# Optimization experiments

Hardware: AMD Instinct MI355X
Metric: run time of the kernel (lower is better)

The kernel has to match this reference:

```python
import jax, jax.numpy as jnp
import numpy as np

B, S, D = 4, 4096, 256
NEG_INF = jnp.float32(-jnp.inf)


def setup_inputs() -> dict:
    key = jax.random.key(0)
    ks = jax.random.split(key, 6)
    x_q = jax.random.normal(ks[0], (B, S, D), dtype=jnp.float32)
    x_k = jax.random.normal(ks[1], (B, S, D), dtype=jnp.float32)
    x_v = jax.random.normal(ks[2], (B, S, D), dtype=jnp.float32)
    attn_mask = jnp.ones((B, S), dtype=jnp.int32)
    # Linear(d_model, d_model, bias=False) weights, torch layout [out, in]
    sc = 1.0 / np.sqrt(D)
    Wq = jax.random.uniform(ks[3], (D, D), minval=-sc, maxval=sc, dtype=jnp.float32)
    Wk = jax.random.uniform(ks[4], (D, D), minval=-sc, maxval=sc, dtype=jnp.float32)
    Wv = jax.random.uniform(ks[5], (D, D), minval=-sc, maxval=sc, dtype=jnp.float32)
    return {"x_q": x_q, "x_k": x_k, "x_v": x_v, "attn_mask": attn_mask,
            "Wq": Wq, "Wk": Wk, "Wv": Wv}


def reference(x_q, x_k, x_v, attn_mask, Wq, Wk, Wv):
    # projections: torch Linear -> x @ W.T
    Q = jnp.einsum('bsd,ed->bse', x_q, Wq)
    K = jnp.einsum('bsd,ed->bse', x_k, Wk)
    V = jnp.einsum('bsd,ed->bse', x_v, Wv)
    d = Q.shape[-1]
    n_q, n_k = Q.shape[1], K.shape[1]
    scale = jnp.sqrt(jnp.float32(d))
    logits = jnp.einsum('bqd,bkd->bqk', Q, K) / scale  # [B, n_q, n_k]
    # causal (mask_future=True)
    causal = jnp.tril(jnp.ones((n_q, n_k), dtype=bool))
    logits = jnp.where(causal[None, :, :], logits, NEG_INF)
    # key padding mask [B, n_k] -> [B, 1, n_k]
    logits = jnp.where(attn_mask[:, None, :] != 0, logits, NEG_INF)
    w = jax.nn.softmax(logits, axis=-1)
    return jnp.einsum('bqk,bkd->bqd', w, V)
```

## Files before the change

### kernel.cpp

```cpp
#include <hip/hip_runtime.h>

#define B_N 4
#define S_LEN 4096
#define D_DIM 256
#define BS_TOT (B_N * S_LEN)
#define BSD_TOT ((size_t)BS_TOT * D_DIM)

typedef __attribute__((ext_vector_type(8))) short short8;
typedef __attribute__((ext_vector_type(4))) short short4_;
typedef __attribute__((ext_vector_type(4))) unsigned short ushort4_;
typedef __attribute__((ext_vector_type(4))) float f32x4;
typedef __attribute__((ext_vector_type(4))) int int4_;

static __device__ __forceinline__ unsigned short f2bf(float f) {
  unsigned u = __builtin_bit_cast(unsigned, f);
  u += 0x7fffu + ((u >> 16) & 1u);
  return (unsigned short)(u >> 16);
}
static __device__ __forceinline__ float bf2f(unsigned short h) {
  unsigned u = ((unsigned)h) << 16;
  return __builtin_bit_cast(float, u);
}

#if __has_builtin(__builtin_amdgcn_mfma_f32_16x16x16bf16_1k)
#define MFMA16(a, b, c) __builtin_amdgcn_mfma_f32_16x16x16bf16_1k((a), (b), (c), 0, 0, 0)
#else
static __device__ __forceinline__ f32x4 mfma16_asm(short4_ a, short4_ b, f32x4 c) {
  asm volatile("v_mfma_f32_16x16x16_bf16 %0, %1, %2, %0" : "+v"(c) : "v"(a), "v"(b));
  return c;
}
#define MFMA16(a, b, c) mfma16_asm((a), (b), (c))
#endif

__global__ __launch_bounds__(256, 2)
void proj_kernel(const float* __restrict__ X0, const float* __restrict__ X1,
                 const float* __restrict__ X2,
                 const float* __restrict__ W0, const float* __restrict__ W1,
                 const float* __restrict__ W2,
                 unsigned short* __restrict__ O0, unsigned short* __restrict__ O1,
                 unsigned short* __restrict__ O2) {
  __shared__ __align__(16) unsigned char sA[16384];
  __shared__ __align__(16) unsigned char sB[16384];

  const int z = (int)blockIdx.z;
  const float* X = (z == 0) ? X0 : (z == 1) ? X1 : X2;
  const float* W = (z == 0) ? W0 : (z == 1) ? W1 : W2;
  unsigned short* O = (z == 0) ? O0 : (z == 1) ? O1 : O2;
  const float mult = (z == 0) ? 0.0625f : 1.0f;

  const int t = (int)threadIdx.x;
  const int l = t & 63, w = t >> 6;
  const int lm = l & 15, g = l >> 4;
  const int wr = w >> 1, wc = w & 1;
  const int mb = (int)blockIdx.x * 128;
  const int nb = (int)blockIdx.y * 128;

  f32x4 acc[4][4];
#pragma unroll
  for (int i = 0; i < 4; ++i)
#pragma unroll
    for (int j = 0; j < 4; ++j) acc[i][j] = (f32x4){0.f, 0.f, 0.f, 0.f};

  for (int ks = 0; ks < 4; ++ks) {
    const int k0 = ks * 64;
#pragma unroll
    for (int i = 0; i < 4; ++i) {
      const int c = t + i * 256;
      const int row = c >> 3;
      const int kc = (c & 7) * 8;
      const float* xp = X + (size_t)(mb + row) * D_DIM + k0 + kc;
      const float* wp = W + (size_t)(nb + row) * D_DIM + k0 + kc;
      f32x4 x0 = *(const f32x4*)xp;
      f32x4 x1 = *(const f32x4*)(xp + 4);
      f32x4 w0 = *(const f32x4*)wp;
      f32x4 w1 = *(const f32x4*)(wp + 4);
      short8 xa, wa;
#pragma unroll
      for (int j = 0; j < 4; ++j) {
        xa[j] = (short)f2bf(x0[j]);
        xa[j + 4] = (short)f2bf(x1[j]);
        wa[j] = (short)f2bf(w0[j]);
        wa[j + 4] = (short)f2bf(w1[j]);
      }
      const int off = row * 128 + ((kc * 2) ^ ((row & 7) << 4));
      *(short8*)&sA[off] = xa;
      *(short8*)&sB[off] = wa;
    }
    __syncthreads();
#pragma unroll
    for (int kk = 0; kk < 2; ++kk) {
      short8 af[4], bg[4];
#pragma unroll
      for (int mi = 0; mi < 4; ++mi) {
        const int row = wr * 64 + mi * 16 + lm;
        af[mi] = *(const short8*)&sA[row * 128 + (((kk * 32 + g * 8) * 2) ^ ((row & 7) << 4))];
      }
#pragma unroll
      for (int ni = 0; ni < 4; ++ni) {
        const int row = wc * 64 + ni * 16 + lm;
        bg[ni] = *(const short8*)&sB[row * 128 + (((kk * 32 + g * 8) * 2) ^ ((row & 7) << 4))];
      }
#pragma unroll
      for (int mi = 0; mi < 4; ++mi)
#pragma unroll
        for (int ni = 0; ni < 4; ++ni)
          acc[mi][ni] = __builtin_amdgcn_mfma_f32_16x16x32_bf16(af[mi], bg[ni], acc[mi][ni], 0, 0, 0);
    }
    __syncthreads();
  }

#pragma unroll
  for (int mi = 0; mi < 4; ++mi)
#pragma unroll
    for (int ni = 0; ni < 4; ++ni)
#pragma unroll
      for (int r = 0; r < 4; ++r) {
        const int mg = mb + wr * 64 + mi * 16 + g * 4 + r;
        const int ng = nb + wc * 64 + ni * 16 + lm;
        O[(size_t)mg * D_DIM + ng] = f2bf(acc[mi][ni][r] * mult);
      }
}

__global__ __launch_bounds__(64)
void mask_flags_kernel(const int* __restrict__ amask, int* __restrict__ flags) {
  const int idx = (int)blockIdx.x * 64 + (int)threadIdx.x;
  const int4_* p = (const int4_*)(amask + (size_t)idx * 64);
  int all1 = 1;
#pragma unroll
  for (int i = 0; i < 16; ++i) {
    int4_ v = p[i];
    all1 &= (v[0] != 0) & (v[1] != 0) & (v[2] != 0) & (v[3] != 0);
  }
  flags[idx] = all1;
}

__global__ __launch_bounds__(512, 2)
void attn_split4_kernel(const unsigned short* __restrict__ Qb,
                        const unsigned short* __restrict__ Kb,
                        const unsigned short* __restrict__ Vb,
                        const int* __restrict__ amask,
                        const int* __restrict__ tflags,
                        unsigned short* __restrict__ Pall,
                        float* __restrict__ stats)
{
  __shared__ __align__(16) unsigned char sBuf[2][65536];

  const int t = (int)threadIdx.x;
  const int l = t & 63;
  const int w = t >> 6;
  const int lm = l & 15;
  const int g = l >> 4;

  const int lin = (int)blockIdx.x;
  const int xcd = lin & 7;
  const int jslot = lin >> 3;
  const int b = xcd >> 1;
  const int slot = (xcd & 1) * 32 + jslot;
  const int pp = slot >> 2;
  const int h = slot & 3;
  const size_t bS = (size_t)b * S_LEN;

  int4_ kreg[4], vreg[4];
  const int crow = t >> 5;
  const int cd8 = (t & 31) << 3;
  const int vko = (crow & 3) * 32 + (crow >> 2) * 8;

#define LOAD_TILE(T0)                                                              \
  do {                                                                             \
    const size_t kb_ = bS + (size_t)((T0)*64);                                     \
    _Pragma("unroll") for (int i_ = 0; i_ < 4; ++i_) {                             \
      kreg[i_] = *(const int4_*)(Kb + (kb_ + crow * 4 + i_) * D_DIM + cd8);        \
      vreg[i_] = *(const int4_*)(Vb + (kb_ + crow * 4 + i_) * D_DIM + cd8);        \
    }                                                                              \
  } while (0)

#define STORE_TILE(BUF)                                                            \
  do {                                                                             \
    unsigned char* bK_ = (BUF);                                                    \
    unsigned char* bV_ = (BUF) + 32768;                                            \
    _Pragma("unroll") for (int i_ = 0; i_ < 4; ++i_) {                             \
      const int row_ = crow * 4 + i_;                                              \
      *(int4_*)&bK_[row_ * 512 + ((cd8 * 2) ^ ((row_ & 7) << 4))] = kreg[i_];      \
    }                                                                              \
    const unsigned short* v0_ = (const unsigned short*)&vreg[0];                   \
    const unsigned short* v1_ = (const unsigned short*)&vreg[1];                   \
    const unsigned short* v2_ = (const unsigned short*)&vreg[2];                   \
    const unsigned short* v3_ = (const unsigned short*)&vreg[3];                   \
    _Pragma("unroll") for (int jj_ = 0; jj_ < 8; ++jj_) {                          \
      const int d_ = cd8 + jj_;                                                    \
      const int sw_ = ((d_ ^ (d_ >> 4)) & 14) << 3;                                \
      short4_ pv_;                                                                 \
      pv_[0] = (short)v0_[jj_]; pv_[1] = (short)v1_[jj_];                          \
      pv_[2] = (short)v2_[jj_]; pv_[3] = (short)v3_[jj_];                          \
      *(short4_*)&bV_[d_ * 128 + (vko ^ sw_)] = pv_;                               \
    }                                                                              \
  } while (0)

  for (int ci = 0; ci < 2; ++ci) {
    const int qc = ci ? (31 - pp) : pp;
    const int last = 2 * qc + 1;
    const int qrow0 = qc * 128;
    const int q_g = qrow0 + w * 16 + lm;

    short8 qf[8];
    {
      const unsigned short* qp = Qb + (bS + (size_t)(qrow0 + w * 16 + lm)) * D_DIM + g * 8;
#pragma unroll
      for (int ch = 0; ch < 8; ++ch) qf[ch] = *(const short8*)(qp + ch * 32);
    }

    f32x4 o[16];
#pragma unroll
    for (int dt = 0; dt < 16; ++dt) o[dt] = (f32x4){0.f, 0.f, 0.f, 0.f};
    float mrun = -1e30f, lrun = 0.f;

    if (h <= last) {
      LOAD_TILE(h);
      STORE_TILE(sBuf[0]);
      if (h + 4 <= last) LOAD_TILE(h + 4);
    }
    __syncthreads();

    int p = 0;
    for (int tt = h; tt <= last; tt += 4) {
      const int k0 = tt * 64;
      const unsigned char* bK = sBuf[p];
      const unsigned char* bV = sBuf[p] + 32768;

      if (tt + 4 <= last) {
        STORE_TILE(sBuf[p ^ 1]);
        if (tt + 8 <= last) LOAD_TILE(tt + 8);
      }

      f32x4 sacc[4];
#pragma unroll
      for (int s = 0; s < 4; ++s) sacc[s] = (f32x4){0.f, 0.f, 0.f, 0.f};
      __builtin_amdgcn_s_setprio(1);
#pragma unroll
      for (int ch = 0; ch < 8; ++ch) {
#pragma unroll
        for (int s = 0; s < 4; ++s) {
          const int key = s * 16 + lm;
          const int off = key * 512 + (((ch * 32 + g * 8) * 2) ^ ((key & 7) << 4));
          short8 kf = *(const short8*)&bK[off];
          sacc[s] = __builtin_amdgcn_mfma_f32_16x16x32_bf16(kf, qf[ch], sacc[s], 0, 0, 0);
        }
      }
      __builtin_amdgcn_s_setprio(0);

      float sv[4][4];
      float tmax = -1e30f;
      const bool fastm = tflags[b * 64 + tt] && (k0 + 63 <= qrow0 + w * 16);
      if (fastm) {
#pragma unroll
        for (int s = 0; s < 4; ++s)
#pragma unroll
          for (int r = 0; r < 4; ++r) {
            sv[s][r] = sacc[s][r];
            tmax = fmaxf(tmax, sacc[s][r]);
          }
      } else {
#pragma unroll
        for (int s = 0; s < 4; ++s) {
          const int4_ mw = *(const int4_*)(amask + bS + k0 + s * 16 + g * 4);
#pragma unroll
          for (int r = 0; r < 4; ++r) {
            const int key_g = k0 + s * 16 + g * 4 + r;
            const bool ok = (key_g <= q_g) && (mw[r] != 0);
            const float x = ok ? sacc[s][r] : -1e30f;
            sv[s][r] = x;
            tmax = fmaxf(tmax, x);
          }
        }
      }
      tmax = fmaxf(tmax, __shfl_xor(tmax, 16));
      tmax = fmaxf(tmax, __shfl_xor(tmax, 32));

      if (__ballot(tmax > mrun)) {
        const float mnew = fmaxf(mrun, tmax);
        const float corr = __builtin_amdgcn_exp2f((mrun - mnew) * 1.44269504f);
        mrun = mnew;
        lrun *= corr;
        float cr[4];
#pragma unroll
        for (int r = 0; r < 4; ++r) cr[r] = __shfl(corr, g * 4 + r);
#pragma unroll
        for (int dt = 0; dt < 16; ++dt)
#pragma unroll
          for (int r = 0; r < 4; ++r) o[dt][r] *= cr[r];
      }

      float psum = 0.f;
      short4_ pk[4];
#pragma unroll
      for (int s = 0; s < 4; ++s) {
#pragma unroll
        for (int r = 0; r < 4; ++r) {
          const float p_ = __builtin_amdgcn_exp2f((sv[s][r] - mrun) * 1.44269504f);
          psum += p_;
          pk[s][r] = (short)f2bf(p_);
        }
      }
      psum += __shfl_xor(psum, 16);
      psum += __shfl_xor(psum, 32);
      lrun += psum;

      __builtin_amdgcn_s_setprio(1);
#pragma unroll
      for (int dt = 0; dt < 16; ++dt) {
        const int d = dt * 16 + lm;
        const int sw = ((d ^ (d >> 4)) & 14) << 3;
        const unsigned char* vr = &bV[d * 128];
        short8 v01 = *(const short8*)&vr[(g * 32) ^ sw];
        short8 v23 = *(const short8*)&vr[(g * 32 + 16) ^ sw];
        short4_ f0 = {v01[0], v01[1], v01[2], v01[3]};
        short4_ f1 = {v01[4], v01[5], v01[6], v01[7]};
        short4_ f2 = {v23[0], v23[1], v23[2], v23[3]};
        short4_ f3 = {v23[4], v23[5], v23[6], v23[7]};
        o[dt] = MFMA16(pk[0], f0, o[dt]);
        o[dt] = MFMA16(pk[1], f1, o[dt]);
        o[dt] = MFMA16(pk[2], f2, o[dt]);
        o[dt] = MFMA16(pk[3], f3, o[dt]);
      }
      __builtin_amdgcn_s_setprio(0);

      __syncthreads();
      p ^= 1;
    }

    unsigned short* op =
        Pall + (size_t)h * BSD_TOT + (bS + (size_t)(qrow0 + w * 16)) * D_DIM;
#pragma unroll
    for (int dt = 0; dt < 16; ++dt)
#pragma unroll
      for (int r = 0; r < 4; ++r)
        op[(size_t)(g * 4 + r) * D_DIM + dt * 16 + lm] = f2bf(o[dt][r]);
    if (g == 0) {
      stats[(size_t)h * BS_TOT + bS + q_g] = mrun;
      stats[(size_t)(4 + h) * BS_TOT + bS + q_g] = lrun;
    }
  }
#undef LOAD_TILE
#undef STORE_TILE
}

__global__ __launch_bounds__(256)
void combine4_kernel(float* __restrict__ Out, const unsigned short* __restrict__ Pall,
                     const float* __restrict__ stats) {
  const int idx = (int)blockIdx.x * 256 + (int)threadIdx.x;
  const int row = idx >> 6;
  const float m0 = stats[row];
  const float m1 = stats[BS_TOT + row];
  const float m2 = stats[2 * BS_TOT + row];
  const float m3 = stats[3 * BS_TOT + row];
  const float mm = fmaxf(fmaxf(m0, m1), fmaxf(m2, m3));
  const float s0 = __builtin_amdgcn_exp2f((m0 - mm) * 1.44269504f);
  const float s1 = __builtin_amdgcn_exp2f((m1 - mm) * 1.44269504f);
  const float s2 = __builtin_amdgcn_exp2f((m2 - mm) * 1.44269504f);
  const float s3 = __builtin_amdgcn_exp2f((m3 - mm) * 1.44269504f);
  const float denom = s0 * stats[4 * BS_TOT + row] + s1 * stats[5 * BS_TOT + row] +
                      s2 * stats[6 * BS_TOT + row] + s3 * stats[7 * BS_TOT + row];
  const float inv = 1.f / denom;

  ushort4_ u0 = *(const ushort4_*)(Pall + (size_t)idx * 4);
  ushort4_ u1 = *(const ushort4_*)(Pall + BSD_TOT + (size_t)idx * 4);
  ushort4_ u2 = *(const ushort4_*)(Pall + 2 * BSD_TOT + (size_t)idx * 4);
  ushort4_ u3 = *(const ushort4_*)(Pall + 3 * BSD_TOT + (size_t)idx * 4);
  f32x4 acc;
#pragma unroll
  for (int j = 0; j < 4; ++j)
    acc[j] = bf2f(u0[j]) * s0 + bf2f(u1[j]) * s1 + bf2f(u2[j]) * s2 + bf2f(u3[j]) * s3;
  *(f32x4*)(Out + (size_t)idx * 4) = acc * inv;
}

__global__ __launch_bounds__(256, 2)
void attn_kernel(const unsigned short* __restrict__ Qb,
                 const unsigned short* __restrict__ Kb,
                 const unsigned short* __restrict__ Vb,
                 const int* __restrict__ amask,
                 float* __restrict__ Out) {
  __shared__ __align__(16) unsigned char sK[32768];
  __shared__ __align__(16) unsigned char sVT[32768];

  const int t = (int)threadIdx.x;
  const int l = t & 63;
  const int w = t >> 6;
  const int lm = l & 15;
  const int g = l >> 4;
  const int b = (int)blockIdx.x >> 6;
  const int qb = (int)blockIdx.x & 63;
  const size_t bS = (size_t)b * S_LEN;

  short8 qf[8];
  {
    const unsigned short* qp = Qb + (bS + (size_t)(qb * 64 + w * 16 + lm)) * D_DIM + g * 8;
#pragma unroll
    for (int ch = 0; ch < 8; ++ch) qf[ch] = *(const short8*)(qp + ch * 32);
  }

  f32x4 o[16];
#pragma unroll
  for (int dt = 0; dt < 16; ++dt) o[dt] = (f32x4){0.f, 0.f, 0.f, 0.f};
  float mrun = -1e30f, lrun = 0.f;
  const int q_g = qb * 64 + w * 16 + lm;

  for (int tt = 0; tt <= qb; ++tt) {
    const int k0 = tt * 64;
#pragma unroll
    for (int i = 0; i < 8; ++i) {
      const int c = t + i * 256;
      const int row = c >> 5;
      const int d8 = (c & 31) << 3;
      {
        int4_ kvv = *(const int4_*)(Kb + (bS + (size_t)(k0 + row)) * D_DIM + d8);
        *(int4_*)&sK[row * 512 + ((d8 * 2) ^ ((row & 7) << 4))] = kvv;
      }
      {
        int4_ vvv = *(const int4_*)(Vb + (bS + (size_t)(k0 + row)) * D_DIM + d8);
        const unsigned short* pv = (const unsigned short*)&vvv;
#pragma unroll
        for (int jj = 0; jj < 8; ++jj) {
          const int d = d8 + jj;
          const int swz = (((d >> 4) ^ d) & 15) << 3;
          *(unsigned short*)&sVT[d * 128 + ((row * 2) ^ swz)] = pv[jj];
        }
      }
    }
    __syncthreads();

    f32x4 sacc[4];
#pragma unroll
    for (int s = 0; s < 4; ++s) sacc[s] = (f32x4){0.f, 0.f, 0.f, 0.f};
#pragma unroll
    for (int ch = 0; ch < 8; ++ch) {
#pragma unroll
      for (int s = 0; s < 4; ++s) {
        const int key = s * 16 + lm;
        const int off = key * 512 + (((ch * 32 + g * 8) * 2) ^ ((key & 7) << 4));
        short8 kf = *(const short8*)&sK[off];
        sacc[s] = __builtin_amdgcn_mfma_f32_16x16x32_bf16(kf, qf[ch], sacc[s], 0, 0, 0);
      }
    }

    float sv[4][4];
    float tmax = -1e30f;
#pragma unroll
    for (int s = 0; s < 4; ++s) {
      const int4_ mw = *(const int4_*)(amask + bS + k0 + s * 16 + g * 4);
#pragma unroll
      for (int r = 0; r < 4; ++r) {
        const int key_g = k0 + s * 16 + g * 4 + r;
        const bool ok = (key_g <= q_g) && (mw[r] != 0);
        const float x = ok ? sacc[s][r] : -1e30f;
        sv[s][r] = x;
        tmax = fmaxf(tmax, x);
      }
    }
    tmax = fmaxf(tmax, __shfl_xor(tmax, 16));
    tmax = fmaxf(tmax, __shfl_xor(tmax, 32));
    const float mnew = fmaxf(mrun, tmax);
    const float corr = __builtin_amdgcn_exp2f((mrun - mnew) * 1.44269504f);
    mrun = mnew;

    float psum = 0.f;
    short4_ pk[4];
#pragma unroll
    for (int s = 0; s < 4; ++s) {
#pragma unroll
      for (int r = 0; r < 4; ++r) {
        const float p = __builtin_amdgcn_exp2f((sv[s][r] - mnew) * 1.44269504f);
        psum += p;
        pk[s][r] = (short)f2bf(p);
      }
    }
    psum += __shfl_xor(psum, 16);
    psum += __shfl_xor(psum, 32);
    lrun = lrun * corr + psum;

    float cr[4];
#pragma unroll
    for (int r = 0; r < 4; ++r) cr[r] = __shfl(corr, g * 4 + r);
#pragma unroll
    for (int dt = 0; dt < 16; ++dt)
#pragma unroll
      for (int r = 0; r < 4; ++r) o[dt][r] *= cr[r];

#pragma unroll
    for (int dt = 0; dt < 16; ++dt) {
      const int d = dt * 16 + lm;
      const int swz = (((d >> 4) ^ d) & 15) << 3;
#pragma unroll
      for (int s = 0; s < 4; ++s) {
        short4_ vf = *(const short4_*)&sVT[d * 128 + ((s * 32 + g * 8) ^ swz)];
        o[dt] = MFMA16(pk[s], vf, o[dt]);
      }
    }
    __syncthreads();
  }

  const float inv = 1.f / lrun;
  float ir[4];
#pragma unroll
  for (int r = 0; r < 4; ++r) ir[r] = __shfl(inv, g * 4 + r);
  float* op = Out + (bS + (size_t)(qb * 64 + w * 16)) * D_DIM;
#pragma unroll
  for (int dt = 0; dt < 16; ++dt)
#pragma unroll
    for (int r = 0; r < 4; ++r)
      op[(size_t)(g * 4 + r) * D_DIM + dt * 16 + lm] = o[dt][r] * ir[r];
}

extern "C" void kernel_launch(void* const* d_in, const int* in_sizes, int n_in,
                              void* d_out, int out_size, void* d_ws, size_t ws_size,
                              hipStream_t stream) {
  const float* x_q = (const float*)d_in[0];
  const float* x_k = (const float*)d_in[1];
  const float* x_v = (const float*)d_in[2];
  const int* amask = (const int*)d_in[3];
  const float* Wq = (const float*)d_in[4];
  const float* Wk = (const float*)d_in[5];
  const float* Wv = (const float*)d_in[6];

  unsigned short* Qb = (unsigned short*)d_ws;
  unsigned short* Kb = Qb + BSD_TOT;
  unsigned short* Vb = Kb + BSD_TOT;

  dim3 pg(128, 2, 3);
  proj_kernel<<<pg, dim3(256), 0, stream>>>(x_q, x_k, x_v, Wq, Wk, Wv, Qb, Kb, Vb);

  const size_t qkv_bytes = 3 * BSD_TOT * sizeof(unsigned short);
  const size_t pall_bytes = 4 * BSD_TOT * sizeof(unsigned short);
  const size_t stat_bytes = 8 * (size_t)BS_TOT * sizeof(float);
  const size_t flag_bytes = (size_t)B_N * 64 * sizeof(int);
  if (ws_size >= qkv_bytes + pall_bytes + stat_bytes + flag_bytes) {
    unsigned short* Pall = (unsigned short*)((char*)d_ws + qkv_bytes);
    float* stats = (float*)((char*)d_ws + qkv_bytes + pall_bytes);
    int* tflags = (int*)((char*)d_ws + qkv_bytes + pall_bytes + stat_bytes);
    mask_flags_kernel<<<dim3(B_N), dim3(64), 0, stream>>>(amask, tflags);
    attn_split4_kernel<<<dim3(256), dim3(512), 0, stream>>>(
        Qb, Kb, Vb, amask, tflags, Pall, stats);
    combine4_kernel<<<dim3((unsigned)(BSD_TOT / 4 / 256)), dim3(256), 0, stream>>>(
        (float*)d_out, Pall, stats);
  } else {
    attn_kernel<<<dim3(B_N * (S_LEN / 64)), dim3(256), 0, stream>>>(Qb, Kb, Vb, amask,
                                                                    (float*)d_out);
  }
}
```

Measured before the change: 100.6 us.

## Retile projection to full-width N tiles and fold mask-flag kernel into it

The projection GEMM now uses 64-row M tiles that span all 256 output columns. Each X row is therefore read and converted to bf16 once rather than once per N block, while each block reloads the full W slice. The separate mask_flags kernel is removed, and its work runs in the first few z==0 projection blocks, saving one launch. The trade-offs are a larger B tile in shared memory, more redundant W traffic, and the fallback path now writing flags into workspace that it may not have sized for.

```diff
diff --git a/kernel.cpp b/kernel.cpp
--- a/kernel.cpp
+++ b/kernel.cpp
@@ -38,9 +38,10 @@
                  const float* __restrict__ W0, const float* __restrict__ W1,
                  const float* __restrict__ W2,
                  unsigned short* __restrict__ O0, unsigned short* __restrict__ O1,
-                 unsigned short* __restrict__ O2) {
-  __shared__ __align__(16) unsigned char sA[16384];
-  __shared__ __align__(16) unsigned char sB[16384];
+                 unsigned short* __restrict__ O2,
+                 const int* __restrict__ amask, int* __restrict__ flags) {
+  __shared__ __align__(16) unsigned char sA[8192];
+  __shared__ __align__(16) unsigned char sB[32768];
 
   const int z = (int)blockIdx.z;
   const float* X = (z == 0) ? X0 : (z == 1) ? X1 : X2;
@@ -51,9 +52,18 @@
   const int t = (int)threadIdx.x;
   const int l = t & 63, w = t >> 6;
   const int lm = l & 15, g = l >> 4;
-  const int wr = w >> 1, wc = w & 1;
-  const int mb = (int)blockIdx.x * 128;
-  const int nb = (int)blockIdx.y * 128;
+  const int mb = (int)blockIdx.x * 64;
+
+  if (z == 0 && (int)blockIdx.x < B_N && t < 64) {
+    const int4_* p = (const int4_*)(amask + ((size_t)blockIdx.x * 64 + t) * 64);
+    int all1 = 1;
+#pragma unroll
+    for (int i = 0; i < 16; ++i) {
+      int4_ v = p[i];
+      all1 &= (v[0] != 0) & (v[1] != 0) & (v[2] != 0) & (v[3] != 0);
+    }
+    flags[(int)blockIdx.x * 64 + t] = all1;
+  }
 
   f32x4 acc[4][4];
 #pragma unroll
@@ -64,27 +74,36 @@
   for (int ks = 0; ks < 4; ++ks) {
     const int k0 = ks * 64;
 #pragma unroll
-    for (int i = 0; i < 4; ++i) {
+    for (int i = 0; i < 2; ++i) {
       const int c = t + i * 256;
       const int row = c >> 3;
       const int kc = (c & 7) * 8;
       const float* xp = X + (size_t)(mb + row) * D_DIM + k0 + kc;
-      const float* wp = W + (size_t)(nb + row) * D_DIM + k0 + kc;
       f32x4 x0 = *(const f32x4*)xp;
       f32x4 x1 = *(const f32x4*)(xp + 4);
-      f32x4 w0 = *(const f32x4*)wp;
-      f32x4 w1 = *(const f32x4*)(wp + 4);
-      short8 xa, wa;
+      short8 xa;
 #pragma unroll
       for (int j = 0; j < 4; ++j) {
         xa[j] = (short)f2bf(x0[j]);
         xa[j + 4] = (short)f2bf(x1[j]);
+      }
+      *(short8*)&sA[row * 128 + ((kc * 2) ^ ((row & 7) << 4))] = xa;
+    }
+#pragma unroll
+    for (int i = 0; i < 8; ++i) {
+      const int c = t + i * 256;
+      const int row = c >> 3;
+      const int kc = (c & 7) * 8;
+      const float* wp = W + (size_t)row * D_DIM + k0 + kc;
+      f32x4 w0 = *(const f32x4*)wp;
+      f32x4 w1 = *(const f32x4*)(wp + 4);
+      short8 wa;
+#pragma unroll
+      for (int j = 0; j < 4; ++j) {
         wa[j] = (short)f2bf(w0[j]);
         wa[j + 4] = (short)f2bf(w1[j]);
       }
-      const int off = row * 128 + ((kc * 2) ^ ((row & 7) << 4));
-      *(short8*)&sA[off] = xa;
-      *(short8*)&sB[off] = wa;
+      *(short8*)&sB[row * 128 + ((kc * 2) ^ ((row & 7) << 4))] = wa;
     }
     __syncthreads();
 #pragma unroll
@@ -92,12 +111,12 @@
       short8 af[4], bg[4];
 #pragma unroll
       for (int mi = 0; mi < 4; ++mi) {
-        const int row = wr * 64 + mi * 16 + lm;
+        const int row = mi * 16 + lm;
         af[mi] = *(const short8*)&sA[row * 128 + (((kk * 32 + g * 8) * 2) ^ ((row & 7) << 4))];
       }
 #pragma unroll
       for (int ni = 0; ni < 4; ++ni) {
-        const int row = wc * 64 + ni * 16 + lm;
+        const int row = w * 64 + ni * 16 + lm;
         bg[ni] = *(const short8*)&sB[row * 128 + (((kk * 32 + g * 8) * 2) ^ ((row & 7) << 4))];
       }
 #pragma unroll
@@ -115,23 +134,10 @@
     for (int ni = 0; ni < 4; ++ni)
 #pragma unroll
       for (int r = 0; r < 4; ++r) {
-        const int mg = mb + wr * 64 + mi * 16 + g * 4 + r;
-        const int ng = nb + wc * 64 + ni * 16 + lm;
+        const int mg = mb + mi * 16 + g * 4 + r;
+        const int ng = w * 64 + ni * 16 + lm;
         O[(size_t)mg * D_DIM + ng] = f2bf(acc[mi][ni][r] * mult);
       }
-}
-
-__global__ __launch_bounds__(64)
-void mask_flags_kernel(const int* __restrict__ amask, int* __restrict__ flags) {
-  const int idx = (int)blockIdx.x * 64 + (int)threadIdx.x;
-  const int4_* p = (const int4_*)(amask + (size_t)idx * 64);
-  int all1 = 1;
-#pragma unroll
-  for (int i = 0; i < 16; ++i) {
-    int4_ v = p[i];
-    all1 &= (v[0] != 0) & (v[1] != 0) & (v[2] != 0) & (v[3] != 0);
-  }
-  flags[idx] = all1;
 }
 
 __global__ __launch_bounds__(512, 2)
@@ -525,9 +531,6 @@
   unsigned short* Kb = Qb + BSD_TOT;
   unsigned short* Vb = Kb + BSD_TOT;
 
-  dim3 pg(128, 2, 3);
-  proj_kernel<<<pg, dim3(256), 0, stream>>>(x_q, x_k, x_v, Wq, Wk, Wv, Qb, Kb, Vb);
-
   const size_t qkv_bytes = 3 * BSD_TOT * sizeof(unsigned short);
   const size_t pall_bytes = 4 * BSD_TOT * sizeof(unsigned short);
   const size_t stat_bytes = 8 * (size_t)BS_TOT * sizeof(float);
@@ -536,12 +539,15 @@
     unsigned short* Pall = (unsigned short*)((char*)d_ws + qkv_bytes);
     float* stats = (float*)((char*)d_ws + qkv_bytes + pall_bytes);
     int* tflags = (int*)((char*)d_ws + qkv_bytes + pall_bytes + stat_bytes);
-    mask_flags_kernel<<<dim3(B_N), dim3(64), 0, stream>>>(amask, tflags);
+    proj_kernel<<<dim3(BS_TOT / 64, 1, 3), dim3(256), 0, stream>>>(
+        x_q, x_k, x_v, Wq, Wk, Wv, Qb, Kb, Vb, amask, tflags);
     attn_split4_kernel<<<dim3(256), dim3(512), 0, stream>>>(
         Qb, Kb, Vb, amask, tflags, Pall, stats);
     combine4_kernel<<<dim3((unsigned)(BSD_TOT / 4 / 256)), dim3(256), 0, stream>>>(
         (float*)d_out, Pall, stats);
   } else {
+    proj_kernel<<<dim3(BS_TOT / 64, 1, 3), dim3(256), 0, stream>>>(
+        x_q, x_k, x_v, Wq, Wk, Wv, Qb, Kb, Vb, amask, (int*)((char*)d_ws + qkv_bytes));
     attn_kernel<<<dim3(B_N * (S_LEN / 64)), dim3(256), 0, stream>>>(Qb, Kb, Vb, amask,
                                                                     (float*)d_out);
   }
```

Result: slower. 104.8 us (+4.2%).

## Fuse split-KV combine into attention kernel via per-tile atomic completion counter

Applied to the files above, without the earlier changes.

Removes the separate combine kernel launch. Each attention block bumps an atomic counter for its query tile after writing its partial output and stats. The last of the four split blocks then merges the partials and writes the final output. This saves a kernel launch and its tail, and may overlap combine work with other blocks' attention, but adds a memset, threadfences, and an uneven combine load on the last-arriving blocks.

```diff
diff --git a/kernel.cpp b/kernel.cpp
--- a/kernel.cpp
+++ b/kernel.cpp
@@ -141,9 +141,12 @@
                         const int* __restrict__ amask,
                         const int* __restrict__ tflags,
                         unsigned short* __restrict__ Pall,
-                        float* __restrict__ stats)
+                        float* __restrict__ stats,
+                        int* __restrict__ cnt,
+                        float* __restrict__ Out)
 {
   __shared__ __align__(16) unsigned char sBuf[2][65536];
+  __shared__ int doComb;
 
   const int t = (int)threadIdx.x;
   const int l = t & 63;
@@ -339,38 +342,53 @@
       stats[(size_t)h * BS_TOT + bS + q_g] = mrun;
       stats[(size_t)(4 + h) * BS_TOT + bS + q_g] = lrun;
     }
+
+    __threadfence();
+    if (t == 0) {
+      const int old = atomicAdd(&cnt[b * 32 + qc], 1);
+      doComb = (old == 3);
+    }
+    __syncthreads();
+    if (doComb) {
+      __threadfence();
+      const int rowl = t >> 2;
+      const int d0 = (t & 3) * 64;
+      const size_t gro = bS + (size_t)(qrow0 + rowl);
+      const float m0 = stats[gro];
+      const float m1 = stats[BS_TOT + gro];
+      const float m2 = stats[2 * BS_TOT + gro];
+      const float m3 = stats[3 * BS_TOT + gro];
+      const float mm = fmaxf(fmaxf(m0, m1), fmaxf(m2, m3));
+      const float s0 = __builtin_amdgcn_exp2f((m0 - mm) * 1.44269504f);
+      const float s1 = __builtin_amdgcn_exp2f((m1 - mm) * 1.44269504f);
+      const float s2 = __builtin_amdgcn_exp2f((m2 - mm) * 1.44269504f);
+      const float s3 = __builtin_amdgcn_exp2f((m3 - mm) * 1.44269504f);
+      const float denom = s0 * stats[4 * BS_TOT + gro] + s1 * stats[5 * BS_TOT + gro] +
+                          s2 * stats[6 * BS_TOT + gro] + s3 * stats[7 * BS_TOT + gro];
+      const float inv = 1.f / denom;
+      const unsigned short* p0 = Pall + gro * D_DIM + d0;
+      const unsigned short* p1 = p0 + BSD_TOT;
+      const unsigned short* p2 = p0 + 2 * BSD_TOT;
+      const unsigned short* p3 = p0 + 3 * BSD_TOT;
+      float* oo = Out + gro * D_DIM + d0;
+#pragma unroll
+      for (int j = 0; j < 16; ++j) {
+        ushort4_ a0 = *(const ushort4_*)(p0 + j * 4);
+        ushort4_ a1 = *(const ushort4_*)(p1 + j * 4);
+        ushort4_ a2 = *(const ushort4_*)(p2 + j * 4);
+        ushort4_ a3 = *(const ushort4_*)(p3 + j * 4);
+        f32x4 acc;
+#pragma unroll
+        for (int jj = 0; jj < 4; ++jj)
+          acc[jj] = bf2f(a0[jj]) * s0 + bf2f(a1[jj]) * s1 + bf2f(a2[jj]) * s2 + bf2f(a3[jj]) * s3;
+        *(f32x4*)oo = acc * inv;
+        oo += 4;
+      }
+    }
+    __syncthreads();
   }
 #undef LOAD_TILE
 #undef STORE_TILE
-}
-
-__global__ __launch_bounds__(256)
-void combine4_kernel(float* __restrict__ Out, const unsigned short* __restrict__ Pall,
-                     const float* __restrict__ stats) {
-  const int idx = (int)blockIdx.x * 256 + (int)threadIdx.x;
-  const int row = idx >> 6;
-  const float m0 = stats[row];
-  const float m1 = stats[BS_TOT + row];
-  const float m2 = stats[2 * BS_TOT + row];
-  const float m3 = stats[3 * BS_TOT + row];
-  const float mm = fmaxf(fmaxf(m0, m1), fmaxf(m2, m3));
-  const float s0 = __builtin_amdgcn_exp2f((m0 - mm) * 1.44269504f);
-  const float s1 = __builtin_amdgcn_exp2f((m1 - mm) * 1.44269504f);
-  const float s2 = __builtin_amdgcn_exp2f((m2 - mm) * 1.44269504f);
-  const float s3 = __builtin_amdgcn_exp2f((m3 - mm) * 1.44269504f);
-  const float denom = s0 * stats[4 * BS_TOT + row] + s1 * stats[5 * BS_TOT + row] +
-                      s2 * stats[6 * BS_TOT + row] + s3 * stats[7 * BS_TOT + row];
-  const float inv = 1.f / denom;
-
-  ushort4_ u0 = *(const ushort4_*)(Pall + (size_t)idx * 4);
-  ushort4_ u1 = *(const ushort4_*)(Pall + BSD_TOT + (size_t)idx * 4);
-  ushort4_ u2 = *(const ushort4_*)(Pall + 2 * BSD_TOT + (size_t)idx * 4);
-  ushort4_ u3 = *(const ushort4_*)(Pall + 3 * BSD_TOT + (size_t)idx * 4);
-  f32x4 acc;
-#pragma unroll
-  for (int j = 0; j < 4; ++j)
-    acc[j] = bf2f(u0[j]) * s0 + bf2f(u1[j]) * s1 + bf2f(u2[j]) * s2 + bf2f(u3[j]) * s3;
-  *(f32x4*)(Out + (size_t)idx * 4) = acc * inv;
 }
 
 __global__ __launch_bounds__(256, 2)
@@ -532,15 +550,16 @@
   const size_t pall_bytes = 4 * BSD_TOT * sizeof(unsigned short);
   const size_t stat_bytes = 8 * (size_t)BS_TOT * sizeof(float);
   const size_t flag_bytes = (size_t)B_N * 64 * sizeof(int);
-  if (ws_size >= qkv_bytes + pall_bytes + stat_bytes + flag_bytes) {
+  const size_t cnt_bytes = (size_t)B_N * 32 * sizeof(int);
+  if (ws_size >= qkv_bytes + pall_bytes + stat_bytes + flag_bytes + cnt_bytes) {
     unsigned short* Pall = (unsigned short*)((char*)d_ws + qkv_bytes);
     float* stats = (float*)((char*)d_ws + qkv_bytes + pall_bytes);
     int* tflags = (int*)((char*)d_ws + qkv_bytes + pall_bytes + stat_bytes);
+    int* cnt = (int*)((char*)d_ws + qkv_bytes + pall_bytes + stat_bytes + flag_bytes);
+    hipMemsetAsync(cnt, 0, cnt_bytes, stream);
     mask_flags_kernel<<<dim3(B_N), dim3(64), 0, stream>>>(amask, tflags);
     attn_split4_kernel<<<dim3(256), dim3(512), 0, stream>>>(
-        Qb, Kb, Vb, amask, tflags, Pall, stats);
-    combine4_kernel<<<dim3((unsigned)(BSD_TOT / 4 / 256)), dim3(256), 0, stream>>>(
-        (float*)d_out, Pall, stats);
+        Qb, Kb, Vb, amask, tflags, Pall, stats, cnt, (float*)d_out);
   } else {
     attn_kernel<<<dim3(B_N * (S_LEN / 64)), dim3(256), 0, stream>>>(Qb, Kb, Vb, amask,
                                                                     (float*)d_out);
```

Result: slower. 282.0 us (+180.4%).
